# Optimization experiments

Measured on AMD Instinct MI355X. Metric: run time of the kernel, lower is better.

## Reference

```python
import jax, jax.numpy as jnp
import numpy as np

WS = 7          # window_size[0]
NUM_HEADS = 8   # hardcoded inside the pooled branch of the torch module
EXPAND = 3     # expand_size
C_DIM = 256


def window_partition(x, ws):
    B, H, W, C = x.shape
    x = x.reshape(B, H // ws, ws, W // ws, ws, C)
    return x.transpose(0, 1, 3, 2, 4, 5).reshape(-1, ws, ws, C)


def setup_inputs() -> dict:
    key = jax.random.key(0)
    ks = jax.random.split(key, 8)
    C = C_DIM
    return {
        "x": jax.random.normal(ks[0], (2, 112, 112, C), jnp.float32),
        "pool0": jax.random.normal(ks[1], (2, 16, 16, 7, 7, C), jnp.float32),
        "clip1": jax.random.normal(ks[2], (2, 16, 16, 7, 7, C), jnp.float32),
        "clip2": jax.random.normal(ks[3], (2, 16, 16, 5, 5, C), jnp.float32),
        "clip3": jax.random.normal(ks[4], (2, 16, 16, 3, 3, C), jnp.float32),
        "qkv_w": jax.random.normal(ks[5], (C, 3 * C), jnp.float32) * 0.02,
        "qkv_b": jnp.zeros((3 * C,), jnp.float32),
        "proj_w": jax.random.normal(ks[6], (C, C), jnp.float32) * 0.02,
        "proj_b": jnp.zeros((C,), jnp.float32),
        "batch_size": 2,
    }


def reference(x, pool0, clip1, clip2, clip3, qkv_w, qkv_b, proj_w, proj_b, batch_size):
    B, H, W, C = x.shape
    nh, hd = NUM_HEADS, C // NUM_HEADS
    scale = hd ** -0.5

    qkv = (x @ qkv_w + qkv_b).reshape(B, H, W, 3, C)
    q, k, v = qkv[..., 0, :], qkv[..., 1, :], qkv[..., 2, :]

    def to_win(t):  # -> (nWB, nh, ws2, hd)
        return window_partition(t, WS).reshape(-1, WS * WS, nh, hd).transpose(0, 2, 1, 3)

    q_w, k_w, v_w = to_win(q), to_win(k), to_win(v)

    shifts = [(-EXPAND, -EXPAND), (-EXPAND, EXPAND), (EXPAND, -EXPAND), (EXPAND, EXPAND)]

    def rolled(t):  # 4 rolled window views, concat on token axis
        parts = [window_partition(jnp.roll(t, s, axis=(1, 2)), WS).reshape(-1, WS * WS, nh, hd)
                 for s in shifts]
        return jnp.concatenate(parts, axis=1).transpose(0, 2, 1, 3)

    k_rolled = jnp.concatenate([k_w, rolled(k)], axis=2)  # (nWB, nh, 5*ws2, hd)
    v_rolled = jnp.concatenate([v_w, rolled(v)], axis=2)

    k_pooled, v_pooled = [], []
    # focal_level-1 == 1 pooled target level: identity copies (NO qkv linear),
    # and the torch code reinterprets (ws2, C) contiguously as (nh, ws2, hd):
    B7, nh7, nw7, wsz, _, d7 = pool0.shape
    t0 = pool0.reshape(B7 * nh7 * nw7, nh, wsz * wsz, d7 // nh)
    k_pooled.append(t0)
    v_pooled.append(t0)

    for clip in (clip1, clip2, clip3):  # focal_l_clips branches: qkv linear applied
        B7, nh7, nw7, wsz, _, d7 = clip.shape
        xw = clip.reshape(B7 * nh7 * nw7, wsz * wsz, d7)
        qkvp = (xw @ qkv_w + qkv_b).reshape(B7 * nh7 * nw7, wsz * wsz, 3, C)
        kk = qkvp[:, :, 1].reshape(-1, wsz * wsz, nh, hd).transpose(0, 2, 1, 3)
        vv = qkvp[:, :, 2].reshape(-1, wsz * wsz, nh, hd).transpose(0, 2, 1, 3)
        k_pooled.append(kk)
        v_pooled.append(vv)

    k_all = jnp.concatenate([k_rolled] + k_pooled, axis=2)  # (nWB, nh, N, hd)
    v_all = jnp.concatenate([v_rolled] + v_pooled, axis=2)

    attn = jnp.einsum('whqd,whkd->whqk', q_w * scale, k_all)
    attn = jax.nn.softmax(attn, axis=-1)
    out = jnp.einsum('whqk,whkd->whqd', attn, v_all)
    out = out.transpose(0, 2, 1, 3).reshape(-1, WS * WS, C)
    return out @ proj_w + proj_b
```

## Files before the change

### kernel.cpp

```cpp
#include <hip/hip_runtime.h>
#include <hip/hip_bf16.h>


#define NKEYS 377

typedef unsigned int u32;
typedef unsigned short u16;
typedef __attribute__((ext_vector_type(8))) short bf16x8;
typedef __attribute__((ext_vector_type(8))) unsigned short u16x8;
typedef __attribute__((ext_vector_type(4))) unsigned int u32x4;
typedef __attribute__((ext_vector_type(2))) unsigned int u32x2;
typedef __attribute__((ext_vector_type(4))) float f32x4;

__device__ __forceinline__ u16 f2bf(float f) {
    u32 b = __float_as_uint(f);
    b += 0x7FFFu + ((b >> 16) & 1u);
    return (u16)(b >> 16);
}
__device__ __forceinline__ u32 pack2(float lo, float hi) {
    return (u32)f2bf(lo) | ((u32)f2bf(hi) << 16);
}
__device__ __forceinline__ bf16x8 cvt8(float4 x, float4 y) {
    union { bf16x8 v; __hip_bfloat162 h[4]; } un;
    un.h[0] = __float22bfloat162_rn(make_float2(x.x, x.y));
    un.h[1] = __float22bfloat162_rn(make_float2(x.z, x.w));
    un.h[2] = __float22bfloat162_rn(make_float2(y.x, y.y));
    un.h[3] = __float22bfloat162_rn(make_float2(y.z, y.w));
    return un.v;
}

__global__ __launch_bounds__(256)
void cvt_kernel(const float* __restrict__ x,  const float* __restrict__ c1,
                const float* __restrict__ c2, const float* __restrict__ c3,
                const float* __restrict__ p0,
                __hip_bfloat16* __restrict__ xb, __hip_bfloat16* __restrict__ c1b,
                __hip_bfloat16* __restrict__ c2b, __hip_bfloat16* __restrict__ c3b,
                __hip_bfloat16* __restrict__ p0b)
{
    const int U0 = 802816, U1 = 1605632, U2 = 2015232, U3 = 2162688, U4 = 2965504;
    for (int u = blockIdx.x * 256 + threadIdx.x; u < U4; u += gridDim.x * 256) {
        const float* s; __hip_bfloat16* d; int o;
        if (u < U0)      { s = x;  d = xb;  o = u; }
        else if (u < U1) { s = c1; d = c1b; o = u - U0; }
        else if (u < U2) { s = c2; d = c2b; o = u - U1; }
        else if (u < U3) { s = c3; d = c3b; o = u - U2; }
        else             { s = p0; d = p0b; o = u - U3; }
        const float4 a = *(const float4*)(s + (size_t)o * 8);
        const float4 b = *(const float4*)(s + (size_t)o * 8 + 4);
        *(bf16x8*)((short*)d + (size_t)o * 8) = cvt8(a, b);
    }
}

__global__ __launch_bounds__(256)
void wprep_kernel(const float* __restrict__ qkv_w,
                  const float* __restrict__ proj_w,
                  __hip_bfloat16* __restrict__ wq,
                  __hip_bfloat16* __restrict__ wp)
{
    const int n = blockIdx.x;
    const int k = threadIdx.x;
    if (n < 768) wq[n * 256 + k] = __float2bfloat16(qkv_w[k * 768 + n]);
    else         wp[(n - 768) * 256 + k] = __float2bfloat16(proj_w[k * 256 + (n - 768)]);
}

#define GLD(gsrc, loff)                                                        \
    __builtin_amdgcn_global_load_lds(                                          \
        (const __attribute__((address_space(1))) void*)(gsrc),                 \
        (__attribute__((address_space(3))) void*)(smem + (loff)), 16, 0, 0)

__global__ __launch_bounds__(256)
void gemm_mfma_kernel(const __hip_bfloat16* __restrict__ A,
                      const __hip_bfloat16* __restrict__ Bt,
                      const float* __restrict__ bias,
                      void* __restrict__ Cv, int ldc, int obf, int nx)
{
    __shared__ __align__(16) char smem[32768];

    const int cpx = gridDim.x >> 3;
    const int bid = blockIdx.x;
    const int bs  = (bid & 7) * cpx + (bid >> 3);
    const int n0  = (bs % nx) * 128;
    const int m0  = (bs / nx) * 128;

    const int tid = threadIdx.x;
    const int lane = tid & 63, wv = tid >> 6;
    const int wm = (wv >> 1) << 6, wn = (wv & 1) << 6;
    const int l15 = lane & 15, g = lane >> 4;

    const int srow = wv * 32 + (lane >> 2);
    const int scol = (lane & 3) << 3;
    const short* Ag = (const short*)A + (size_t)(m0 + srow) * 256 + scol;
    const short* Bg = (const short*)Bt + (size_t)(n0 + srow) * 256 + scol;

    f32x4 acc[4][4];
    const f32x4 z4 = {0.f, 0.f, 0.f, 0.f};
#pragma unroll
    for (int i = 0; i < 4; ++i)
#pragma unroll
        for (int j = 0; j < 4; ++j) acc[i][j] = z4;

    auto stage = [&](int buf, int k0) {
        const int b0 = buf * 16384 + wv * 2048;
        GLD(Ag + k0,            b0);
        GLD(Ag + k0 + 16 * 256, b0 + 1024);
        GLD(Bg + k0,            b0 + 8192);
        GLD(Bg + k0 + 16 * 256, b0 + 8192 + 1024);
    };

    stage(0, 0);
    __syncthreads();
    int cur = 0;
    for (int kt = 0; kt < 8; ++kt) {
        if (kt < 7) stage(cur ^ 1, (kt + 1) * 32);
        const char* Ab = smem + cur * 16384;
        const char* Bb = Ab + 8192;
        bf16x8 af[4], bfr[4];
#pragma unroll
        for (int rb = 0; rb < 4; ++rb)
            af[rb] = *(const bf16x8*)(Ab + (wm + rb * 16 + l15) * 64 + g * 16);
#pragma unroll
        for (int cb = 0; cb < 4; ++cb)
            bfr[cb] = *(const bf16x8*)(Bb + (wn + cb * 16 + l15) * 64 + g * 16);
#pragma unroll
        for (int rb = 0; rb < 4; ++rb)
#pragma unroll
            for (int cb = 0; cb < 4; ++cb)
                acc[rb][cb] = __builtin_amdgcn_mfma_f32_16x16x32_bf16(
                    bfr[cb], af[rb], acc[rb][cb], 0, 0, 0);
        __syncthreads();
        cur ^= 1;
    }

    float4 b4[4];
#pragma unroll
    for (int cb = 0; cb < 4; ++cb)
        b4[cb] = *(const float4*)(bias + n0 + wn + cb * 16 + (g << 2));
    if (obf) {
        __hip_bfloat16* C = (__hip_bfloat16*)Cv;
#pragma unroll
        for (int rb = 0; rb < 4; ++rb) {
            const int m = m0 + wm + rb * 16 + l15;
            __hip_bfloat16* crow = C + (size_t)m * ldc + n0 + wn + (g << 2);
#pragma unroll
            for (int cb = 0; cb < 4; ++cb) {
                u32x2 pk;
                pk[0] = pack2(acc[rb][cb][0] + b4[cb].x, acc[rb][cb][1] + b4[cb].y);
                pk[1] = pack2(acc[rb][cb][2] + b4[cb].z, acc[rb][cb][3] + b4[cb].w);
                *(u32x2*)(crow + cb * 16) = pk;
            }
        }
    } else {
        float* C = (float*)Cv;
#pragma unroll
        for (int rb = 0; rb < 4; ++rb) {
            const int m = m0 + wm + rb * 16 + l15;
            float* crow = C + (size_t)m * ldc + n0 + wn + (g << 2);
#pragma unroll
            for (int cb = 0; cb < 4; ++cb) {
                float4 o;
                o.x = acc[rb][cb][0] + b4[cb].x;
                o.y = acc[rb][cb][1] + b4[cb].y;
                o.z = acc[rb][cb][2] + b4[cb].z;
                o.w = acc[rb][cb][3] + b4[cb].w;
                *(float4*)(crow + cb * 16) = o;
            }
        }
    }
}

#define VT_OFF   0
#define KL_OFF   24576
#define SMAX_OFF 49152
#define SSUM_OFF 50176
#define GMAX_OFF 51200
#define PBUF_OFF 24576
#define ORED_OFF 0
#define LDS_SZ   51456

__global__ __launch_bounds__(256)
void attn_kernel(const __hip_bfloat16* __restrict__ qkvb,
                 const __hip_bfloat16* __restrict__ pool0b,
                 const __hip_bfloat16* __restrict__ kv1b,
                 const __hip_bfloat16* __restrict__ kv2b,
                 const __hip_bfloat16* __restrict__ kv3b,
                 __hip_bfloat16* __restrict__ outb)
{
    __shared__ __align__(16) char smem[LDS_SZ];

    const int bid = blockIdx.x;
    const int wh  = (bid & 7) * 512 + (bid >> 3);
    const int win = wh >> 3, h = wh & 7;
    const int bb  = win >> 8, wi = (win >> 4) & 15, wj = win & 15;
    const int tid = threadIdx.x;
    const int lane = tid & 63, ww = tid >> 6;
    const int l15 = lane & 15, g = lane >> 4;
    const short* qkv = (const short*)qkvb;

    bf16x8 aq[4];
    const bf16x8 zb = {0, 0, 0, 0, 0, 0, 0, 0};
#pragma unroll
    for (int rb = 0; rb < 4; ++rb) {
        const int r16 = rb * 16 + l15;
        if (r16 < 49) {
            const int aa = r16 / 7, cc = r16 % 7;
            const int row = (bb * 112 + wi * 7 + aa) * 112 + wj * 7 + cc;
            aq[rb] = *(const bf16x8*)(qkv + (size_t)row * 768 + h * 32 + g * 8);
        } else aq[rb] = zb;
    }

    if (tid < 192) {
        const int j0   = tid * 2;
        const int gw   = j0 / 96, rem = j0 % 96;
        const int gk   = rem / 32, gl = (rem % 32) >> 1;
        const int keyA = (gw * 6 + gk * 2) * 16 + gl;
        u16x8 vb[2][4];
#pragma unroll
        for (int s = 0; s < 2; ++s) {
            const int key = keyA + s * 16;
            if (key < NKEYS) {
                const short *kp, *vp;
                if (key < 245) {
                    int aa, cc, hh, ww2;
                    if (key < 49) {
                        aa = key / 7; cc = key % 7;
                        hh = wi * 7 + aa; ww2 = wj * 7 + cc;
                    } else {
                        const int u = key - 49, si = u / 49, rr = u % 49;
                        aa = rr / 7; cc = rr % 7;
                        const int sh = (si < 2) ? -3 : 3;
                        const int sw = (si & 1) ? 3 : -3;
                        hh  = (wi * 7 + aa - sh + 112) % 112;
                        ww2 = (wj * 7 + cc - sw + 112) % 112;
                    }
                    const int row = (bb * 112 + hh) * 112 + ww2;
                    kp = qkv + (size_t)row * 768 + 256 + h * 32;
                    vp = qkv + (size_t)row * 768 + 512 + h * 32;
                } else if (key < 294) {
                    const short* p = (const short*)pool0b + (size_t)win * 12544 + h * 1568 + (key - 245) * 32;
                    kp = p; vp = p;
                } else if (key < 343) {
                    const short* p = (const short*)kv1b + (size_t)(win * 49 + key - 294) * 512 + h * 32;
                    kp = p; vp = p + 256;
                } else if (key < 368) {
                    const short* p = (const short*)kv2b + (size_t)(win * 25 + key - 343) * 512 + h * 32;
                    kp = p; vp = p + 256;
                } else {
                    const short* p = (const short*)kv3b + (size_t)(win * 9 + key - 368) * 512 + h * 32;
                    kp = p; vp = p + 256;
                }
                const u16x8* kp4 = (const u16x8*)kp;
                const u16x8* vp4 = (const u16x8*)vp;
#pragma unroll
                for (int jq = 0; jq < 4; ++jq)
                    *(u16x8*)(smem + KL_OFF + jq * 6144 + key * 16) = kp4[jq];
#pragma unroll
                for (int jq = 0; jq < 4; ++jq) vb[s][jq] = vp4[jq];
            } else {
                const u16x8 z = {0, 0, 0, 0, 0, 0, 0, 0};
#pragma unroll
                for (int jq = 0; jq < 4; ++jq)
                    *(u16x8*)(smem + KL_OFF + jq * 6144 + key * 16) = z;
#pragma unroll
                for (int jq = 0; jq < 4; ++jq) vb[s][jq] = z;
            }
        }
#pragma unroll
        for (int d = 0; d < 32; ++d) {
            int byte = d * 768 + tid * 4;
            byte ^= (d & 7) << 4;
            const u32 lo = vb[0][d >> 3][d & 7];
            const u32 hi = vb[1][d >> 3][d & 7];
            *(u32*)(smem + VT_OFF + byte) = lo | (hi << 16);
        }
    }
    __syncthreads();

    f32x4 S[4][6];
    const f32x4 z4 = {0.f, 0.f, 0.f, 0.f};
#pragma unroll
    for (int c = 0; c < 6; ++c) {
        const int key = (ww * 6 + c) * 16 + l15;
        const bf16x8 bk = *(const bf16x8*)(smem + KL_OFF + g * 6144 + key * 16);
#pragma unroll
        for (int rb = 0; rb < 4; ++rb)
            S[rb][c] = __builtin_amdgcn_mfma_f32_16x16x32_bf16(aq[rb], bk, z4, 0, 0, 0);
    }

    float mx[4][4];
#pragma unroll
    for (int rb = 0; rb < 4; ++rb)
#pragma unroll
        for (int r = 0; r < 4; ++r) {
            float v = S[rb][0][r];
#pragma unroll
            for (int c = 1; c < 6; ++c) v = fmaxf(v, S[rb][c][r]);
            mx[rb][r] = v;
        }
#pragma unroll
    for (int mvar = 1; mvar <= 8; mvar <<= 1)
#pragma unroll
        for (int rb = 0; rb < 4; ++rb)
#pragma unroll
            for (int r = 0; r < 4; ++r)
                mx[rb][r] = fmaxf(mx[rb][r], __shfl_xor(mx[rb][r], mvar, 64));
    {
        const int drb = l15 >> 2, dr = l15 & 3;
        const int row = 16 * drb + 4 * g + dr;
        *(float*)(smem + SMAX_OFF + (ww * 64 + row) * 4) = mx[drb][dr];
    }
    __syncthreads();

    if (tid < 64) {
        float gmv = *(const float*)(smem + SMAX_OFF + tid * 4);
#pragma unroll
        for (int wv2 = 1; wv2 < 4; ++wv2)
            gmv = fmaxf(gmv, *(const float*)(smem + SMAX_OFF + (wv2 * 64 + tid) * 4));
        *(float*)(smem + GMAX_OFF + tid * 4) = gmv;
    }
    __syncthreads();

    float gm[4][4];
#pragma unroll
    for (int rb = 0; rb < 4; ++rb)
#pragma unroll
        for (int r = 0; r < 4; ++r)
            gm[rb][r] = *(const float*)(smem + GMAX_OFF + (16 * rb + 4 * g + r) * 4);

    const float scale = 0.17677669529663687f;
    float sm[4][4];
#pragma unroll
    for (int rb = 0; rb < 4; ++rb)
#pragma unroll
        for (int r = 0; r < 4; ++r) sm[rb][r] = 0.f;

#pragma unroll
    for (int c = 0; c < 6; ++c) {
        const bool tail = (ww == 3) && (c == 5) && (l15 >= 9);
#pragma unroll
        for (int rb = 0; rb < 4; ++rb) {
            f32x4 p;
#pragma unroll
            for (int r = 0; r < 4; ++r) {
                const float e = tail ? 0.f : __expf((S[rb][c][r] - gm[rb][r]) * scale);
                p[r] = e;
                sm[rb][r] += e;
            }
            S[rb][c] = p;
        }
    }
#pragma unroll
    for (int mvar = 1; mvar <= 8; mvar <<= 1)
#pragma unroll
        for (int rb = 0; rb < 4; ++rb)
#pragma unroll
            for (int r = 0; r < 4; ++r)
                sm[rb][r] += __shfl_xor(sm[rb][r], mvar, 64);
    {
        const int drb = l15 >> 2, dr = l15 & 3;
        const int row = 16 * drb + 4 * g + dr;
        *(float*)(smem + SSUM_OFF + (ww * 64 + row) * 4) = sm[drb][dr];
    }

    f32x4 O_[4][2];
#pragma unroll
    for (int rb = 0; rb < 4; ++rb) { O_[rb][0] = z4; O_[rb][1] = z4; }

    char* pbuf = smem + PBUF_OFF + ww * 5120;
#pragma unroll
    for (int kcl = 0; kcl < 3; ++kcl) {
#pragma unroll
        for (int rb = 0; rb < 4; ++rb)
#pragma unroll
            for (int r = 0; r < 4; ++r) {
                const int row = 16 * rb + 4 * g + r;
                *(u32*)(pbuf + row * 80 + l15 * 4) =
                    pack2(S[rb][2 * kcl][r], S[rb][2 * kcl + 1][r]);
            }
        bf16x8 bv[2];
#pragma unroll
        for (int nc = 0; nc < 2; ++nc) {
            const int dim = 16 * nc + l15;
            int byte = dim * 768 + ww * 192 + kcl * 64 + g * 16;
            byte ^= (dim & 7) << 4;
            bv[nc] = *(const bf16x8*)(smem + VT_OFF + byte);
        }
#pragma unroll
        for (int rb = 0; rb < 4; ++rb) {
            const bf16x8 ap = *(const bf16x8*)(pbuf + (16 * rb + l15) * 80 + g * 16);
            O_[rb][0] = __builtin_amdgcn_mfma_f32_16x16x32_bf16(ap, bv[0], O_[rb][0], 0, 0, 0);
            O_[rb][1] = __builtin_amdgcn_mfma_f32_16x16x32_bf16(ap, bv[1], O_[rb][1], 0, 0, 0);
        }
    }
    __syncthreads();

#pragma unroll
    for (int rb = 0; rb < 4; ++rb)
#pragma unroll
        for (int nc = 0; nc < 2; ++nc)
#pragma unroll
            for (int r = 0; r < 4; ++r) {
                const int row = 16 * rb + 4 * g + r;
                const int col = 16 * nc + l15;
                *(float*)(smem + ORED_OFF + ((ww * 64 + row) * 33 + col) * 4) = O_[rb][nc][r];
            }
    __syncthreads();

    {
        const int row = tid >> 2, d0 = (tid & 3) * 8;
        if (row < 49) {
            float lt = 0.f;
#pragma unroll
            for (int wv2 = 0; wv2 < 4; ++wv2)
                lt += *(const float*)(smem + SSUM_OFF + (wv2 * 64 + row) * 4);
            const float inv = 1.0f / lt;
            float o[8];
#pragma unroll
            for (int i = 0; i < 8; ++i) {
                float s = 0.f;
#pragma unroll
                for (int wv2 = 0; wv2 < 4; ++wv2)
                    s += *(const float*)(smem + ORED_OFF + ((wv2 * 64 + row) * 33 + d0 + i) * 4);
                o[i] = s * inv;
            }
            u32x4 pk;
#pragma unroll
            for (int i = 0; i < 4; ++i) pk[i] = pack2(o[2 * i], o[2 * i + 1]);
            *(u32x4*)((short*)outb + (size_t)(win * 49 + row) * 256 + h * 32 + d0) = pk;
        }
    }
}

extern "C" void kernel_launch(void* const* d_in, const int* in_sizes, int n_in,
                              void* d_out, int out_size, void* d_ws, size_t ws_size,
                              hipStream_t stream)
{
    const float* x      = (const float*)d_in[0];
    const float* pool0  = (const float*)d_in[1];
    const float* clip1  = (const float*)d_in[2];
    const float* clip2  = (const float*)d_in[3];
    const float* clip3  = (const float*)d_in[4];
    const float* qkv_w  = (const float*)d_in[5];
    const float* qkv_b  = (const float*)d_in[6];
    const float* proj_w = (const float*)d_in[7];
    const float* proj_b = (const float*)d_in[8];
    float* out = (float*)d_out;

    __hip_bfloat16* ws  = (__hip_bfloat16*)d_ws;
    __hip_bfloat16* qkvb = ws;
    __hip_bfloat16* kv1b = qkvb + 25088ull * 768;
    __hip_bfloat16* kv2b = kv1b + 25088ull * 512;
    __hip_bfloat16* kv3b = kv2b + 12800ull * 512;
    __hip_bfloat16* attnb = kv3b + 4608ull * 512;
    __hip_bfloat16* xb   = attnb + 25088ull * 256;
    __hip_bfloat16* c1b  = xb + 25088ull * 256;
    __hip_bfloat16* c2b  = c1b + 25088ull * 256;
    __hip_bfloat16* c3b  = c2b + 12800ull * 256;
    __hip_bfloat16* p0b  = c3b + 4608ull * 256;
    __hip_bfloat16* wq   = p0b + 512ull * 12544;
    __hip_bfloat16* wp   = wq + 768ull * 256;

    cvt_kernel<<<dim3(2048), dim3(256), 0, stream>>>(
        x, clip1, clip2, clip3, pool0, xb, c1b, c2b, c3b, p0b);
    wprep_kernel<<<dim3(1024), dim3(256), 0, stream>>>(qkv_w, proj_w, wq, wp);

    gemm_mfma_kernel<<<dim3(1176), dim3(256), 0, stream>>>(
        xb, wq, qkv_b, qkvb, 768, 1, 6);
    gemm_mfma_kernel<<<dim3(1328), dim3(256), 0, stream>>>(
        c1b, wq + 256 * 256, qkv_b + 256, kv1b, 512, 1, 4);
    attn_kernel<<<dim3(512 * 8), dim3(256), 0, stream>>>(
        qkvb, p0b, kv1b, kv2b, kv3b, attnb);
    gemm_mfma_kernel<<<dim3(392), dim3(256), 0, stream>>>(
        attnb, wp, proj_b, out, 256, 0, 2);
}
```

Baseline: 299.6 us.

## Merge weight prep into convert kernel, fuse QKV GEMMs, split attention launch

Folds the weight transpose/convert into the input conversion kernel and merges the two QKV projection GEMMs into one launch that dispatches tiles by block index. The attention kernel is split into two half-size launches with a base offset. The intent is fewer kernel launches and less tail idling between the GEMM phases. The split attention launch adds a launch and changes the block-to-window mapping, which may hurt cache locality.

```diff
diff --git a/kernel.cpp b/kernel.cpp
--- a/kernel.cpp
+++ b/kernel.cpp
@@ -30,12 +30,14 @@
 }
 
 __global__ __launch_bounds__(256)
-void cvt_kernel(const float* __restrict__ x,  const float* __restrict__ c1,
-                const float* __restrict__ c2, const float* __restrict__ c3,
-                const float* __restrict__ p0,
-                __hip_bfloat16* __restrict__ xb, __hip_bfloat16* __restrict__ c1b,
-                __hip_bfloat16* __restrict__ c2b, __hip_bfloat16* __restrict__ c3b,
-                __hip_bfloat16* __restrict__ p0b)
+void cvtw_kernel(const float* __restrict__ x,  const float* __restrict__ c1,
+                 const float* __restrict__ c2, const float* __restrict__ c3,
+                 const float* __restrict__ p0,
+                 const float* __restrict__ qkv_w, const float* __restrict__ proj_w,
+                 __hip_bfloat16* __restrict__ xb, __hip_bfloat16* __restrict__ c1b,
+                 __hip_bfloat16* __restrict__ c2b, __hip_bfloat16* __restrict__ c3b,
+                 __hip_bfloat16* __restrict__ p0b,
+                 __hip_bfloat16* __restrict__ wq, __hip_bfloat16* __restrict__ wp)
 {
     const int U0 = 802816, U1 = 1605632, U2 = 2015232, U3 = 2162688, U4 = 2965504;
     for (int u = blockIdx.x * 256 + threadIdx.x; u < U4; u += gridDim.x * 256) {
@@ -49,18 +51,11 @@
         const float4 b = *(const float4*)(s + (size_t)o * 8 + 4);
         *(bf16x8*)((short*)d + (size_t)o * 8) = cvt8(a, b);
     }
-}
-
-__global__ __launch_bounds__(256)
-void wprep_kernel(const float* __restrict__ qkv_w,
-                  const float* __restrict__ proj_w,
-                  __hip_bfloat16* __restrict__ wq,
-                  __hip_bfloat16* __restrict__ wp)
-{
-    const int n = blockIdx.x;
-    const int k = threadIdx.x;
-    if (n < 768) wq[n * 256 + k] = __float2bfloat16(qkv_w[k * 768 + n]);
-    else         wp[(n - 768) * 256 + k] = __float2bfloat16(proj_w[k * 256 + (n - 768)]);
+    for (int u = blockIdx.x * 256 + threadIdx.x; u < 262144; u += gridDim.x * 256) {
+        const int n = u >> 8, k = u & 255;
+        if (n < 768) wq[n * 256 + k] = __float2bfloat16(qkv_w[k * 768 + n]);
+        else         wp[(n - 768) * 256 + k] = __float2bfloat16(proj_w[k * 256 + (n - 768)]);
+    }
 }
 
 #define GLD(gsrc, loff)                                                        \
@@ -68,20 +63,13 @@
         (const __attribute__((address_space(1))) void*)(gsrc),                 \
         (__attribute__((address_space(3))) void*)(smem + (loff)), 16, 0, 0)
 
-__global__ __launch_bounds__(256)
-void gemm_mfma_kernel(const __hip_bfloat16* __restrict__ A,
-                      const __hip_bfloat16* __restrict__ Bt,
-                      const float* __restrict__ bias,
-                      void* __restrict__ Cv, int ldc, int obf, int nx)
+__device__ __forceinline__
+void gemm_tile(const __hip_bfloat16* __restrict__ A,
+               const __hip_bfloat16* __restrict__ Bt,
+               const float* __restrict__ bias,
+               void* __restrict__ Cv, int ldc, int obf,
+               int m0, int n0, char* smem)
 {
-    __shared__ __align__(16) char smem[32768];
-
-    const int cpx = gridDim.x >> 3;
-    const int bid = blockIdx.x;
-    const int bs  = (bid & 7) * cpx + (bid >> 3);
-    const int n0  = (bs % nx) * 128;
-    const int m0  = (bs / nx) * 128;
-
     const int tid = threadIdx.x;
     const int lane = tid & 63, wv = tid >> 6;
     const int wm = (wv >> 1) << 6, wn = (wv & 1) << 6;
@@ -168,6 +156,41 @@
     }
 }
 
+__global__ __launch_bounds__(256)
+void gemm_fused_kernel(const __hip_bfloat16* __restrict__ xb,
+                       const __hip_bfloat16* __restrict__ c1b,
+                       const __hip_bfloat16* __restrict__ wq,
+                       const float* __restrict__ qkv_b,
+                       __hip_bfloat16* __restrict__ qkvb,
+                       __hip_bfloat16* __restrict__ kv1b)
+{
+    __shared__ __align__(16) char smem[32768];
+    const int cpx = gridDim.x >> 3;
+    const int bid = blockIdx.x;
+    const int bs  = (bid & 7) * cpx + (bid >> 3);
+    if (bs < 1176) {
+        gemm_tile(xb, wq, qkv_b, qkvb, 768, 1,
+                  (bs / 6) * 128, (bs % 6) * 128, smem);
+    } else {
+        const int b2 = bs - 1176;
+        gemm_tile(c1b, wq + 256 * 256, qkv_b + 256, kv1b, 512, 1,
+                  (b2 / 4) * 128, (b2 % 4) * 128, smem);
+    }
+}
+
+__global__ __launch_bounds__(256)
+void gemm_mfma_kernel(const __hip_bfloat16* __restrict__ A,
+                      const __hip_bfloat16* __restrict__ Bt,
+                      const float* __restrict__ bias,
+                      void* __restrict__ Cv, int ldc, int obf, int nx)
+{
+    __shared__ __align__(16) char smem[32768];
+    const int cpx = gridDim.x >> 3;
+    const int bid = blockIdx.x;
+    const int bs  = (bid & 7) * cpx + (bid >> 3);
+    gemm_tile(A, Bt, bias, Cv, ldc, obf, (bs / nx) * 128, (bs % nx) * 128, smem);
+}
+
 #define VT_OFF   0
 #define KL_OFF   24576
 #define SMAX_OFF 49152
@@ -183,12 +206,13 @@
                  const __hip_bfloat16* __restrict__ kv1b,
                  const __hip_bfloat16* __restrict__ kv2b,
                  const __hip_bfloat16* __restrict__ kv3b,
-                 __hip_bfloat16* __restrict__ outb)
+                 __hip_bfloat16* __restrict__ outb,
+                 int whbase)
 {
     __shared__ __align__(16) char smem[LDS_SZ];
 
     const int bid = blockIdx.x;
-    const int wh  = (bid & 7) * 512 + (bid >> 3);
+    const int wh  = whbase + ((bid & 7) << 8) + (bid >> 3);
     const int win = wh >> 3, h = wh & 7;
     const int bb  = win >> 8, wi = (win >> 4) & 15, wj = win & 15;
     const int tid = threadIdx.x;
@@ -459,16 +483,18 @@
     __hip_bfloat16* wq   = p0b + 512ull * 12544;
     __hip_bfloat16* wp   = wq + 768ull * 256;
 
-    cvt_kernel<<<dim3(2048), dim3(256), 0, stream>>>(
-        x, clip1, clip2, clip3, pool0, xb, c1b, c2b, c3b, p0b);
-    wprep_kernel<<<dim3(1024), dim3(256), 0, stream>>>(qkv_w, proj_w, wq, wp);
-
-    gemm_mfma_kernel<<<dim3(1176), dim3(256), 0, stream>>>(
-        xb, wq, qkv_b, qkvb, 768, 1, 6);
-    gemm_mfma_kernel<<<dim3(1328), dim3(256), 0, stream>>>(
-        c1b, wq + 256 * 256, qkv_b + 256, kv1b, 512, 1, 4);
-    attn_kernel<<<dim3(512 * 8), dim3(256), 0, stream>>>(
-        qkvb, p0b, kv1b, kv2b, kv3b, attnb);
+    cvtw_kernel<<<dim3(2048), dim3(256), 0, stream>>>(
+        x, clip1, clip2, clip3, pool0, qkv_w, proj_w,
+        xb, c1b, c2b, c3b, p0b, wq, wp);
+
+    gemm_fused_kernel<<<dim3(2504), dim3(256), 0, stream>>>(
+        xb, c1b, wq, qkv_b, qkvb, kv1b);
+
+    attn_kernel<<<dim3(2048), dim3(256), 0, stream>>>(
+        qkvb, p0b, kv1b, kv2b, kv3b, attnb, 0);
+    attn_kernel<<<dim3(2048), dim3(256), 0, stream>>>(
+        qkvb, p0b, kv1b, kv2b, kv3b, attnb, 2048);
+
     gemm_mfma_kernel<<<dim3(392), dim3(256), 0, stream>>>(
         attnb, wp, proj_b, out, 256, 0, 2);
 }
```

Result: no change. 295.4 us (-1.4%).
